# Performance work log

Hardware: AMD Instinct MI355X
Metric: run time of the kernel (lower is better)

Reference implementation:

```python
import jax, jax.numpy as jnp
import numpy as np

# Instant-NGP HashEncoder defaults (torch-ngp) with desired_resolution=2048
L = 16            # num levels
F = 2             # features per level
T = 2 ** 19       # hashmap size per level
BASE = 16         # base resolution
DESIRED = 2048
BOUND = 1.0
PLS = float(np.exp(np.log(DESIRED / BASE) / (L - 1)))
RES = [int(np.ceil(BASE * PLS ** l)) for l in range(L)]  # per-level grid resolution

_OFFS = jnp.array([[i, j, k] for i in range(2) for j in range(2) for k in range(2)], dtype=jnp.uint32)  # [8,3]
_P1 = jnp.uint32(2654435761)
_P2 = jnp.uint32(805459861)


def _level_encode(x01, table, res):
    """x01: [N,3] in [0,1]; table: [T,F]; returns trilinearly-interpolated [N,F]."""
    pos = x01 * res                      # [N,3]
    pf = jnp.floor(pos)
    frac = pos - pf                      # [N,3]
    pi = pf.astype(jnp.uint32)
    corners = pi[:, None, :] + _OFFS[None]  # [N,8,3]
    if (res + 1) ** 3 <= T:
        # dense (collision-free) indexing for coarse levels
        s = jnp.uint32(res + 1)
        idx = corners[..., 0] + s * (corners[..., 1] + s * corners[..., 2])
    else:
        # spatial hash: xor of coordinate * large primes, masked to table size
        idx = (corners[..., 0] ^ (corners[..., 1] * _P1) ^ (corners[..., 2] * _P2)) & jnp.uint32(T - 1)
    # trilinear weights: prod over dims of frac (offset=1) or 1-frac (offset=0)
    w = jnp.prod(jnp.where(_OFFS[None].astype(bool), frac[:, None, :], 1.0 - frac[:, None, :]), axis=-1)  # [N,8]
    return jnp.sum(table[idx] * w[..., None], axis=1)  # [N,F]


def setup_inputs() -> dict:
    key = jax.random.key(0)
    k1, k2, k3, k4 = jax.random.split(key, 4)
    N = 2_097_152
    xyzs = jax.random.uniform(k1, (N, 3), jnp.float32) * 2.0 - 1.0          # in [-bound, bound]
    tables = (jax.random.uniform(k2, (L, T, F), jnp.float32) * 2.0 - 1.0) * 1e-4  # NGP init U(-1e-4,1e-4)
    W1 = jax.random.normal(k3, (L * F, 64), jnp.float32) * (1.0 / np.sqrt(L * F))
    W2 = jax.random.normal(k4, (64, 16), jnp.float32) * (1.0 / np.sqrt(64.0))
    return {"xyzs": xyzs, "tables": tables, "W1": W1, "W2": W2}


def reference(xyzs, tables, W1, W2):
    # normalize to [0,1] using bound (encoder(xyzs, bound))
    x01 = jnp.clip((xyzs + BOUND) / (2.0 * BOUND), 0.0, 1.0)
    enc = jnp.concatenate([_level_encode(x01, tables[l], RES[l]) for l in range(L)], axis=-1)  # [N,32]
    h = jax.nn.relu(enc @ W1)   # [N,64]
    out = h @ W2                # [N,16]
    sigmas = jnp.exp(out[..., 0])   # trunc_exp activation on density channel
    geo_features = out[..., 1:]     # [N,15]
    return sigmas, geo_features
```

## Files before the change

kernel.cpp:

```cpp
#include <hip/hip_runtime.h>
#include <math.h>

#define NLEV 16
#define TSIZE 524288
#define TMASK (TSIZE - 1)
#define P1 2654435761u
#define P2 805459861u

struct ResParams { int res[NLEV]; int dense[NLEV]; };

__device__ __forceinline__ float clamp01f(float v) {
    return fminf(fmaxf(v, 0.0f), 1.0f);
}

__device__ __forceinline__ unsigned f2bf(float f) {
    union { float f; unsigned u; } c; c.f = f;
    return (c.u + 0x7FFFu + ((c.u >> 16) & 1u)) >> 16;
}
__device__ __forceinline__ float bflo(unsigned u) {
    union { unsigned u; float f; } c; c.u = u << 16; return c.f;
}
__device__ __forceinline__ float bfhi(unsigned u) {
    union { unsigned u; float f; } c; c.u = u & 0xFFFF0000u; return c.f;
}

__global__ __launch_bounds__(256) void prep_kernel(
    const float* __restrict__ tables,
    const float* __restrict__ W1,
    const float* __restrict__ W2,
    unsigned* __restrict__ tbl_bf,
    float* __restrict__ W1t,
    float* __restrict__ W2c)
{
    const int t = blockIdx.x * 256 + threadIdx.x;
    const float4 v = *(const float4*)(tables + (size_t)t * 4);
    uint2 o;
    o.x = f2bf(v.x) | (f2bf(v.y) << 16);
    o.y = f2bf(v.z) | (f2bf(v.w) << 16);
    *(uint2*)(tbl_bf + (size_t)t * 2) = o;

    if (blockIdx.x == 0) {
        for (int i = threadIdx.x; i < 2048; i += 256)
            W1t[(i & 63) * 32 + (i >> 6)] = W1[i];
        for (int i = threadIdx.x; i < 1024; i += 256)
            W2c[i] = W2[i];
    }
}

__global__ __launch_bounds__(256) void enc_dense_kernel(
    const float* __restrict__ xyzs,
    const float* __restrict__ tables,
    unsigned* __restrict__ enc_ws,
    ResParams rp, int N)
{
    const int gid = blockIdx.x * 256 + threadIdx.x;
    const float x0 = clamp01f((__builtin_nontemporal_load(xyzs + 3 * gid + 0) + 1.0f) * 0.5f);
    const float y0 = clamp01f((__builtin_nontemporal_load(xyzs + 3 * gid + 1) + 1.0f) * 0.5f);
    const float z0 = clamp01f((__builtin_nontemporal_load(xyzs + 3 * gid + 2) + 1.0f) * 0.5f);
    const float2* tb = (const float2*)tables;

#pragma unroll
    for (int l = 0; l < 5; ++l) {
        const int res = rp.res[l];
        const float rf = (float)res;
        const float px = x0 * rf, py = y0 * rf, pz = z0 * rf;
        const float fx = floorf(px), fy = floorf(py), fz = floorf(pz);
        const float rx = px - fx, ry = py - fy, rz = pz - fz;
        const unsigned ix = (unsigned)fx, iy = (unsigned)fy, iz = (unsigned)fz;

        const unsigned s = (unsigned)(res + 1);
        const unsigned ss = s * s;
        const unsigned base = ix + s * (iy + s * iz);
        unsigned idx[8];
        idx[0] = base;
        idx[1] = base + ss;
        idx[2] = base + s;
        idx[3] = base + s + ss;
        idx[4] = base + 1u;
        idx[5] = base + 1u + ss;
        idx[6] = base + 1u + s;
        idx[7] = base + 1u + s + ss;

        const float2* tl = tb + (size_t)l * TSIZE;
        float2 v[8];
#pragma unroll
        for (int c = 0; c < 8; ++c) v[c] = tl[idx[c]];

        const float wx0 = 1.0f - rx, wy0 = 1.0f - ry, wz0 = 1.0f - rz;
        float e0 = 0.0f, e1 = 0.0f;
#pragma unroll
        for (int c = 0; c < 8; ++c) {
            const float wx = (c & 4) ? rx : wx0;
            const float wy = (c & 2) ? ry : wy0;
            const float wz = (c & 1) ? rz : wz0;
            const float w = (wx * wy) * wz;
            e0 += w * v[c].x;
            e1 += w * v[c].y;
        }
        __builtin_nontemporal_store(f2bf(e0) | (f2bf(e1) << 16),
                                    enc_ws + (size_t)l * N + gid);
    }
}

__global__ __launch_bounds__(256) void enc_hash_kernel(
    const float* __restrict__ xyzs,
    const unsigned* __restrict__ tbl_bf,
    unsigned* __restrict__ enc_ws,
    int level, int res, int N)
{
    const int gid = blockIdx.x * 256 + threadIdx.x;
    const float x0 = clamp01f((__builtin_nontemporal_load(xyzs + 3 * gid + 0) + 1.0f) * 0.5f);
    const float y0 = clamp01f((__builtin_nontemporal_load(xyzs + 3 * gid + 1) + 1.0f) * 0.5f);
    const float z0 = clamp01f((__builtin_nontemporal_load(xyzs + 3 * gid + 2) + 1.0f) * 0.5f);

    const float rf = (float)res;
    const float px = x0 * rf, py = y0 * rf, pz = z0 * rf;
    const float fx = floorf(px), fy = floorf(py), fz = floorf(pz);
    const float rx = px - fx, ry = py - fy, rz = pz - fz;
    const unsigned ix = (unsigned)fx, iy = (unsigned)fy, iz = (unsigned)fz;

    const unsigned ax0 = ix,        ax1 = ix + 1u;
    const unsigned by0 = iy * P1,   by1 = (iy + 1u) * P1;
    const unsigned cz0 = iz * P2,   cz1 = (iz + 1u) * P2;
    unsigned idx[8];
    idx[0] = (ax0 ^ by0 ^ cz0) & TMASK;
    idx[1] = (ax0 ^ by0 ^ cz1) & TMASK;
    idx[2] = (ax0 ^ by1 ^ cz0) & TMASK;
    idx[3] = (ax0 ^ by1 ^ cz1) & TMASK;
    idx[4] = (ax1 ^ by0 ^ cz0) & TMASK;
    idx[5] = (ax1 ^ by0 ^ cz1) & TMASK;
    idx[6] = (ax1 ^ by1 ^ cz0) & TMASK;
    idx[7] = (ax1 ^ by1 ^ cz1) & TMASK;

    const unsigned* tl = tbl_bf + (size_t)level * TSIZE;
    unsigned v[8];
#pragma unroll
    for (int c = 0; c < 8; ++c) v[c] = tl[idx[c]];

    const float wx0 = 1.0f - rx, wy0 = 1.0f - ry, wz0 = 1.0f - rz;
    float e0 = 0.0f, e1 = 0.0f;
#pragma unroll
    for (int c = 0; c < 8; ++c) {
        const float wx = (c & 4) ? rx : wx0;
        const float wy = (c & 2) ? ry : wy0;
        const float wz = (c & 1) ? rz : wz0;
        const float w = (wx * wy) * wz;
        e0 += w * bflo(v[c]);
        e1 += w * bfhi(v[c]);
    }
    __builtin_nontemporal_store(f2bf(e0) | (f2bf(e1) << 16),
                                enc_ws + (size_t)level * N + gid);
}

__global__ __launch_bounds__(256) void mlp_kernel(
    const unsigned* __restrict__ enc_ws,
    const float* __restrict__ W1t,
    const float* __restrict__ W2c,
    float* __restrict__ out_sigma,
    float* __restrict__ out_geo,
    int N)
{
    __shared__ float sGeo[4 * 128 * 15];

    const int tid  = threadIdx.x;
    const int wave = tid >> 6;
    const int lane = tid & 63;
    const int base = blockIdx.x * 512 + wave * 128;
    const int pt0 = base + lane;
    const int pt1 = base + 64 + lane;

    float ea[32], eb[32];
#pragma unroll
    for (int l = 0; l < NLEV; ++l) {
        const unsigned u0 = __builtin_nontemporal_load(enc_ws + (size_t)l * N + pt0);
        const unsigned u1 = __builtin_nontemporal_load(enc_ws + (size_t)l * N + pt1);
        ea[2 * l] = bflo(u0); ea[2 * l + 1] = bfhi(u0);
        eb[2 * l] = bflo(u1); eb[2 * l + 1] = bfhi(u1);
    }

    float oa[16], ob[16];
#pragma unroll
    for (int q = 0; q < 16; ++q) { oa[q] = 0.0f; ob[q] = 0.0f; }

#pragma unroll 4
    for (int j = 0; j < 64; ++j) {
        const float4* wr = (const float4*)(W1t + j * 32);
        float h0 = 0.0f, h1 = 0.0f;
#pragma unroll
        for (int k = 0; k < 8; ++k) {
            const float4 w = wr[k];
            h0 += ea[4 * k + 0] * w.x; h1 += eb[4 * k + 0] * w.x;
            h0 += ea[4 * k + 1] * w.y; h1 += eb[4 * k + 1] * w.y;
            h0 += ea[4 * k + 2] * w.z; h1 += eb[4 * k + 2] * w.z;
            h0 += ea[4 * k + 3] * w.w; h1 += eb[4 * k + 3] * w.w;
        }
        h0 = fmaxf(h0, 0.0f); h1 = fmaxf(h1, 0.0f);
        const float4* w2 = (const float4*)(W2c + j * 16);
#pragma unroll
        for (int q = 0; q < 4; ++q) {
            const float4 w = w2[q];
            oa[4 * q + 0] += h0 * w.x; ob[4 * q + 0] += h1 * w.x;
            oa[4 * q + 1] += h0 * w.y; ob[4 * q + 1] += h1 * w.y;
            oa[4 * q + 2] += h0 * w.z; ob[4 * q + 2] += h1 * w.z;
            oa[4 * q + 3] += h0 * w.w; ob[4 * q + 3] += h1 * w.w;
        }
    }

    out_sigma[pt0] = expf(oa[0]);
    out_sigma[pt1] = expf(ob[0]);

    float* gs = &sGeo[wave * 1920];
#pragma unroll
    for (int q = 1; q < 16; ++q) gs[lane * 15 + (q - 1)] = oa[q];
#pragma unroll
    for (int q = 1; q < 16; ++q) gs[(64 + lane) * 15 + (q - 1)] = ob[q];
    __syncthreads();
    const size_t wbase = (size_t)base * 15;
#pragma unroll
    for (int j = 0; j < 30; ++j)
        out_geo[wbase + (size_t)(j * 64 + lane)] = gs[j * 64 + lane];
}

__global__ __launch_bounds__(256) void hashgrid_fused_kernel(
    const float* __restrict__ xyzs,
    const float* __restrict__ tables,
    const float* __restrict__ W1,
    const float* __restrict__ W2,
    float* __restrict__ out_sigma,
    float* __restrict__ out_geo,
    ResParams rp)
{
    __shared__ float sW1t[64 * 32];
    __shared__ float sW2[64 * 16];
    __shared__ float sGeo[256 * 15];

    const int tid = threadIdx.x;
    for (int i = tid; i < 2048; i += 256) {
        int k = i >> 6, j = i & 63;
        sW1t[j * 32 + k] = W1[i];
    }
    for (int i = tid; i < 1024; i += 256) sW2[i] = W2[i];
    __syncthreads();

    const int gid = blockIdx.x * 256 + tid;
    const float x0 = clamp01f((xyzs[3 * gid + 0] + 1.0f) * 0.5f);
    const float y0 = clamp01f((xyzs[3 * gid + 1] + 1.0f) * 0.5f);
    const float z0 = clamp01f((xyzs[3 * gid + 2] + 1.0f) * 0.5f);

    float enc[32];
    const float2* tb = (const float2*)tables;

#pragma unroll
    for (int l = 0; l < NLEV; ++l) {
        const int res = rp.res[l];
        const float rf = (float)res;
        const float px = x0 * rf, py = y0 * rf, pz = z0 * rf;
        const float fx = floorf(px), fy = floorf(py), fz = floorf(pz);
        const float rx = px - fx, ry = py - fy, rz = pz - fz;
        const unsigned ix = (unsigned)fx, iy = (unsigned)fy, iz = (unsigned)fz;

        unsigned idx[8];
        if (rp.dense[l]) {
            const unsigned s = (unsigned)(res + 1);
            const unsigned ss = s * s;
            const unsigned base = ix + s * (iy + s * iz);
            idx[0] = base;          idx[1] = base + ss;
            idx[2] = base + s;      idx[3] = base + s + ss;
            idx[4] = base + 1u;     idx[5] = base + 1u + ss;
            idx[6] = base + 1u + s; idx[7] = base + 1u + s + ss;
        } else {
            const unsigned ax0 = ix,        ax1 = ix + 1u;
            const unsigned by0 = iy * P1,   by1 = (iy + 1u) * P1;
            const unsigned cz0 = iz * P2,   cz1 = (iz + 1u) * P2;
            idx[0] = (ax0 ^ by0 ^ cz0) & TMASK;
            idx[1] = (ax0 ^ by0 ^ cz1) & TMASK;
            idx[2] = (ax0 ^ by1 ^ cz0) & TMASK;
            idx[3] = (ax0 ^ by1 ^ cz1) & TMASK;
            idx[4] = (ax1 ^ by0 ^ cz0) & TMASK;
            idx[5] = (ax1 ^ by0 ^ cz1) & TMASK;
            idx[6] = (ax1 ^ by1 ^ cz0) & TMASK;
            idx[7] = (ax1 ^ by1 ^ cz1) & TMASK;
        }

        const float2* tl = tb + (size_t)l * TSIZE;
        float2 v[8];
#pragma unroll
        for (int c = 0; c < 8; ++c) v[c] = tl[idx[c]];

        const float wx0 = 1.0f - rx, wy0 = 1.0f - ry, wz0 = 1.0f - rz;
        float e0 = 0.0f, e1 = 0.0f;
#pragma unroll
        for (int c = 0; c < 8; ++c) {
            const float wx = (c & 4) ? rx : wx0;
            const float wy = (c & 2) ? ry : wy0;
            const float wz = (c & 1) ? rz : wz0;
            const float w = (wx * wy) * wz;
            e0 += w * v[c].x;
            e1 += w * v[c].y;
        }
        enc[2 * l]     = e0;
        enc[2 * l + 1] = e1;
    }

    float outv[16];
#pragma unroll
    for (int q = 0; q < 16; ++q) outv[q] = 0.0f;

    for (int j = 0; j < 64; ++j) {
        const float4* wrow = (const float4*)&sW1t[j * 32];
        float hj = 0.0f;
#pragma unroll
        for (int kk = 0; kk < 8; ++kk) {
            const float4 wv = wrow[kk];
            hj += enc[4 * kk + 0] * wv.x;
            hj += enc[4 * kk + 1] * wv.y;
            hj += enc[4 * kk + 2] * wv.z;
            hj += enc[4 * kk + 3] * wv.w;
        }
        hj = fmaxf(hj, 0.0f);
        const float4* w2row = (const float4*)&sW2[j * 16];
#pragma unroll
        for (int qq = 0; qq < 4; ++qq) {
            const float4 w2v = w2row[qq];
            outv[4 * qq + 0] += hj * w2v.x;
            outv[4 * qq + 1] += hj * w2v.y;
            outv[4 * qq + 2] += hj * w2v.z;
            outv[4 * qq + 3] += hj * w2v.w;
        }
    }

    out_sigma[gid] = expf(outv[0]);

    const int wave = tid >> 6;
    const int lane = tid & 63;
    float* gs = &sGeo[wave * 960];
#pragma unroll
    for (int q = 1; q < 16; ++q) gs[lane * 15 + (q - 1)] = outv[q];
    __syncthreads();
    const size_t wbase = (size_t)(blockIdx.x * 256 + wave * 64) * 15;
#pragma unroll
    for (int j = 0; j < 15; ++j)
        out_geo[wbase + (size_t)(j * 64 + lane)] = gs[j * 64 + lane];
}

extern "C" void kernel_launch(void* const* d_in, const int* in_sizes, int n_in,
                              void* d_out, int out_size, void* d_ws, size_t ws_size,
                              hipStream_t stream) {
    const float* xyzs   = (const float*)d_in[0];
    const float* tables = (const float*)d_in[1];
    const float* W1     = (const float*)d_in[2];
    const float* W2     = (const float*)d_in[3];
    float* out = (float*)d_out;

    const int N = in_sizes[0] / 3;

    ResParams rp;
    const double PLS = exp(log(2048.0 / 16.0) / 15.0);
    for (int l = 0; l < NLEV; ++l) {
        const double r = ceil(16.0 * pow(PLS, (double)l));
        rp.res[l] = (int)r;
        const long long s = (long long)r + 1;
        rp.dense[l] = (s * s * s <= (long long)TSIZE) ? 1 : 0;
    }
    bool pattern_ok = true;
    for (int l = 0; l < NLEV; ++l)
        if (rp.dense[l] != (l < 5 ? 1 : 0)) pattern_ok = false;

    float* out_sigma = out;
    float* out_geo   = out + N;

    const size_t encB = (size_t)NLEV * (size_t)N * 4;
    const size_t tblB = (size_t)NLEV * (size_t)TSIZE * 4;
    const size_t w1B  = 2048 * 4, w2B = 1024 * 4;
    const size_t need = encB + tblB + w1B + w2B;

    if (pattern_ok && ws_size >= need) {
        unsigned* enc_ws = (unsigned*)d_ws;
        unsigned* tbl_bf = (unsigned*)((char*)d_ws + encB);
        float*    W1t    = (float*)((char*)d_ws + encB + tblB);
        float*    W2c    = (float*)((char*)d_ws + encB + tblB + w1B);

        prep_kernel<<<dim3((NLEV * TSIZE * 2) / 4 / 256), dim3(256), 0, stream>>>(
            tables, W1, W2, tbl_bf, W1t, W2c);

        const dim3 grid(N / 256), block(256);
        enc_dense_kernel<<<grid, block, 0, stream>>>(xyzs, tables, enc_ws, rp, N);
        for (int l = 5; l < NLEV; ++l)
            enc_hash_kernel<<<grid, block, 0, stream>>>(
                xyzs, tbl_bf, enc_ws, l, rp.res[l], N);

        mlp_kernel<<<dim3(N / 512), block, 0, stream>>>(
            enc_ws, W1t, W2c, out_sigma, out_geo, N);
    } else {
        hashgrid_fused_kernel<<<dim3(N / 256), dim3(256), 0, stream>>>(
            xyzs, tables, W1, W2, out_sigma, out_geo, rp);
    }
}
```

Measured before the change: 1.429 ms.

## Morton-sort points before encoding to improve hash-table gather locality

Adds a counting sort of input points by a 15-bit Morton key (histogram, scan, atomic scatter) so the encoding kernels process spatially coherent points and reuse cached table lines. Dense levels now use a precomputed x-adjacent float4 pair table, halving gather count. Hash kernels process two points per thread. The MLP stages weights in shared memory and scatters outputs through the permutation. This adds sort passes and uncoalesced output writes in exchange for better cache locality on the random gathers.

```diff
diff --git a/kernel.cpp b/kernel.cpp
--- a/kernel.cpp
+++ b/kernel.cpp
@@ -6,13 +6,17 @@
 #define TMASK (TSIZE - 1)
 #define P1 2654435761u
 #define P2 805459861u
-
-struct ResParams { int res[NLEV]; int dense[NLEV]; };
+#define NB 32768
+
+struct Params {
+    int res[NLEV];
+    unsigned ncell[5];
+    unsigned doff[5];
+};
 
 __device__ __forceinline__ float clamp01f(float v) {
     return fminf(fmaxf(v, 0.0f), 1.0f);
 }
-
 __device__ __forceinline__ unsigned f2bf(float f) {
     union { float f; unsigned u; } c; c.f = f;
     return (c.u + 0x7FFFu + ((c.u >> 16) & 1u)) >> 16;
@@ -22,6 +26,16 @@
 }
 __device__ __forceinline__ float bfhi(unsigned u) {
     union { unsigned u; float f; } c; c.u = u & 0xFFFF0000u; return c.f;
+}
+__device__ __forceinline__ unsigned spread5(unsigned v) {
+    return (v & 1u) | ((v & 2u) << 2) | ((v & 4u) << 4) |
+           ((v & 8u) << 6) | ((v & 16u) << 8);
+}
+__device__ __forceinline__ unsigned morton_key(float x0, float y0, float z0) {
+    unsigned kx = min(31u, (unsigned)(x0 * 32.0f));
+    unsigned ky = min(31u, (unsigned)(y0 * 32.0f));
+    unsigned kz = min(31u, (unsigned)(z0 * 32.0f));
+    return spread5(kx) | (spread5(ky) << 1) | (spread5(kz) << 2);
 }
 
 __global__ __launch_bounds__(256) void prep_kernel(
@@ -29,16 +43,21 @@
     const float* __restrict__ W1,
     const float* __restrict__ W2,
     unsigned* __restrict__ tbl_bf,
-    float* __restrict__ W1t,
-    float* __restrict__ W2c)
-{
-    const int t = blockIdx.x * 256 + threadIdx.x;
-    const float4 v = *(const float4*)(tables + (size_t)t * 4);
-    uint2 o;
-    o.x = f2bf(v.x) | (f2bf(v.y) << 16);
-    o.y = f2bf(v.z) | (f2bf(v.w) << 16);
-    *(uint2*)(tbl_bf + (size_t)t * 2) = o;
-
+    float4* __restrict__ dense_pairs,
+    float* __restrict__ W1t, float* __restrict__ W2c,
+    Params rp)
+{
+    const unsigned t = blockIdx.x * 256 + threadIdx.x;
+    const unsigned l = t >> 19, c = t & TMASK;
+    const float2* t2 = (const float2*)tables;
+    if (l >= 5) {
+        const float2 v = t2[(size_t)l * TSIZE + c];
+        tbl_bf[(size_t)(l - 5) * TSIZE + c] = f2bf(v.x) | (f2bf(v.y) << 16);
+    } else if (c < rp.ncell[l]) {
+        const float2 a = t2[(size_t)l * TSIZE + c];
+        const float2 b = t2[(size_t)l * TSIZE + c + 1];
+        dense_pairs[rp.doff[l] + c] = make_float4(a.x, a.y, b.x, b.y);
+    }
     if (blockIdx.x == 0) {
         for (int i = threadIdx.x; i < 2048; i += 256)
             W1t[(i & 63) * 32 + (i >> 6)] = W1[i];
@@ -47,17 +66,62 @@
     }
 }
 
-__global__ __launch_bounds__(256) void enc_dense_kernel(
-    const float* __restrict__ xyzs,
-    const float* __restrict__ tables,
+__global__ __launch_bounds__(256) void zero_kernel(unsigned* __restrict__ hist) {
+    hist[blockIdx.x * 256 + threadIdx.x] = 0u;
+}
+
+__global__ __launch_bounds__(256) void hist_kernel(
+    const float* __restrict__ xyzs, unsigned* __restrict__ hist)
+{
+    const int gid = blockIdx.x * 256 + threadIdx.x;
+    const float x0 = clamp01f((xyzs[3 * gid + 0] + 1.0f) * 0.5f);
+    const float y0 = clamp01f((xyzs[3 * gid + 1] + 1.0f) * 0.5f);
+    const float z0 = clamp01f((xyzs[3 * gid + 2] + 1.0f) * 0.5f);
+    atomicAdd(&hist[morton_key(x0, y0, z0)], 1u);
+}
+
+__global__ __launch_bounds__(1024) void scan_kernel(
+    const unsigned* __restrict__ hist, unsigned* __restrict__ work)
+{
+    __shared__ unsigned part[1024];
+    const int tid = threadIdx.x;
+    unsigned loc[32], s = 0;
+#pragma unroll
+    for (int i = 0; i < 32; ++i) { loc[i] = hist[tid * 32 + i]; s += loc[i]; }
+    part[tid] = s; __syncthreads();
+    for (int st = 1; st < 1024; st <<= 1) {
+        unsigned t = (tid >= st) ? part[tid - st] : 0u;
+        __syncthreads();
+        part[tid] += t;
+        __syncthreads();
+    }
+    unsigned base = (tid == 0) ? 0u : part[tid - 1];
+#pragma unroll
+    for (int i = 0; i < 32; ++i) { work[tid * 32 + i] = base; base += loc[i]; }
+}
+
+__global__ __launch_bounds__(256) void scatter_kernel(
+    const float* __restrict__ xyzs, unsigned* __restrict__ work,
+    float4* __restrict__ sorted, unsigned* __restrict__ perm)
+{
+    const int gid = blockIdx.x * 256 + threadIdx.x;
+    const float x0 = clamp01f((xyzs[3 * gid + 0] + 1.0f) * 0.5f);
+    const float y0 = clamp01f((xyzs[3 * gid + 1] + 1.0f) * 0.5f);
+    const float z0 = clamp01f((xyzs[3 * gid + 2] + 1.0f) * 0.5f);
+    const unsigned pos = atomicAdd(&work[morton_key(x0, y0, z0)], 1u);
+    sorted[pos] = make_float4(x0, y0, z0, 0.0f);
+    perm[pos] = (unsigned)gid;
+}
+
+__global__ __launch_bounds__(256) void enc_dense_sorted(
+    const float4* __restrict__ sorted,
+    const float4* __restrict__ dense_pairs,
     unsigned* __restrict__ enc_ws,
-    ResParams rp, int N)
+    Params rp, int N)
 {
     const int gid = blockIdx.x * 256 + threadIdx.x;
-    const float x0 = clamp01f((__builtin_nontemporal_load(xyzs + 3 * gid + 0) + 1.0f) * 0.5f);
-    const float y0 = clamp01f((__builtin_nontemporal_load(xyzs + 3 * gid + 1) + 1.0f) * 0.5f);
-    const float z0 = clamp01f((__builtin_nontemporal_load(xyzs + 3 * gid + 2) + 1.0f) * 0.5f);
-    const float2* tb = (const float2*)tables;
+    const float4 p = sorted[gid];
+    const float x0 = p.x, y0 = p.y, z0 = p.z;
 
 #pragma unroll
     for (int l = 0; l < 5; ++l) {
@@ -70,104 +134,104 @@
 
         const unsigned s = (unsigned)(res + 1);
         const unsigned ss = s * s;
-        const unsigned base = ix + s * (iy + s * iz);
-        unsigned idx[8];
-        idx[0] = base;
-        idx[1] = base + ss;
-        idx[2] = base + s;
-        idx[3] = base + s + ss;
-        idx[4] = base + 1u;
-        idx[5] = base + 1u + ss;
-        idx[6] = base + 1u + s;
-        idx[7] = base + 1u + s + ss;
-
-        const float2* tl = tb + (size_t)l * TSIZE;
-        float2 v[8];
-#pragma unroll
-        for (int c = 0; c < 8; ++c) v[c] = tl[idx[c]];
+        const unsigned a = ix + s * iy + ss * iz;
+        const float4* dpt = dense_pairs + rp.doff[l];
+        const float4 q00 = dpt[a];
+        const float4 q01 = dpt[a + ss];
+        const float4 q10 = dpt[a + s];
+        const float4 q11 = dpt[a + s + ss];
 
         const float wx0 = 1.0f - rx, wy0 = 1.0f - ry, wz0 = 1.0f - rz;
-        float e0 = 0.0f, e1 = 0.0f;
-#pragma unroll
-        for (int c = 0; c < 8; ++c) {
-            const float wx = (c & 4) ? rx : wx0;
-            const float wy = (c & 2) ? ry : wy0;
-            const float wz = (c & 1) ? rz : wz0;
-            const float w = (wx * wy) * wz;
-            e0 += w * v[c].x;
-            e1 += w * v[c].y;
-        }
+        float e0, e1;
+        e0  = (wx0 * wy0) * wz0 * q00.x;  e1  = (wx0 * wy0) * wz0 * q00.y;
+        e0 += (wx0 * wy0) * rz  * q01.x;  e1 += (wx0 * wy0) * rz  * q01.y;
+        e0 += (wx0 * ry ) * wz0 * q10.x;  e1 += (wx0 * ry ) * wz0 * q10.y;
+        e0 += (wx0 * ry ) * rz  * q11.x;  e1 += (wx0 * ry ) * rz  * q11.y;
+        e0 += (rx  * wy0) * wz0 * q00.z;  e1 += (rx  * wy0) * wz0 * q00.w;
+        e0 += (rx  * wy0) * rz  * q01.z;  e1 += (rx  * wy0) * rz  * q01.w;
+        e0 += (rx  * ry ) * wz0 * q10.z;  e1 += (rx  * ry ) * wz0 * q10.w;
+        e0 += (rx  * ry ) * rz  * q11.z;  e1 += (rx  * ry ) * rz  * q11.w;
+
         __builtin_nontemporal_store(f2bf(e0) | (f2bf(e1) << 16),
                                     enc_ws + (size_t)l * N + gid);
     }
 }
 
-__global__ __launch_bounds__(256) void enc_hash_kernel(
-    const float* __restrict__ xyzs,
+template<int LEVEL>
+__global__ __launch_bounds__(256) void enc_hash_sorted(
+    const float4* __restrict__ sorted,
     const unsigned* __restrict__ tbl_bf,
     unsigned* __restrict__ enc_ws,
-    int level, int res, int N)
-{
-    const int gid = blockIdx.x * 256 + threadIdx.x;
-    const float x0 = clamp01f((__builtin_nontemporal_load(xyzs + 3 * gid + 0) + 1.0f) * 0.5f);
-    const float y0 = clamp01f((__builtin_nontemporal_load(xyzs + 3 * gid + 1) + 1.0f) * 0.5f);
-    const float z0 = clamp01f((__builtin_nontemporal_load(xyzs + 3 * gid + 2) + 1.0f) * 0.5f);
-
+    int res, int N)
+{
+    const int g0 = blockIdx.x * 512 + threadIdx.x;
+    const unsigned* tl = tbl_bf + (size_t)(LEVEL - 5) * TSIZE;
     const float rf = (float)res;
-    const float px = x0 * rf, py = y0 * rf, pz = z0 * rf;
-    const float fx = floorf(px), fy = floorf(py), fz = floorf(pz);
-    const float rx = px - fx, ry = py - fy, rz = pz - fz;
-    const unsigned ix = (unsigned)fx, iy = (unsigned)fy, iz = (unsigned)fz;
-
-    const unsigned ax0 = ix,        ax1 = ix + 1u;
-    const unsigned by0 = iy * P1,   by1 = (iy + 1u) * P1;
-    const unsigned cz0 = iz * P2,   cz1 = (iz + 1u) * P2;
-    unsigned idx[8];
-    idx[0] = (ax0 ^ by0 ^ cz0) & TMASK;
-    idx[1] = (ax0 ^ by0 ^ cz1) & TMASK;
-    idx[2] = (ax0 ^ by1 ^ cz0) & TMASK;
-    idx[3] = (ax0 ^ by1 ^ cz1) & TMASK;
-    idx[4] = (ax1 ^ by0 ^ cz0) & TMASK;
-    idx[5] = (ax1 ^ by0 ^ cz1) & TMASK;
-    idx[6] = (ax1 ^ by1 ^ cz0) & TMASK;
-    idx[7] = (ax1 ^ by1 ^ cz1) & TMASK;
-
-    const unsigned* tl = tbl_bf + (size_t)level * TSIZE;
-    unsigned v[8];
-#pragma unroll
-    for (int c = 0; c < 8; ++c) v[c] = tl[idx[c]];
-
-    const float wx0 = 1.0f - rx, wy0 = 1.0f - ry, wz0 = 1.0f - rz;
-    float e0 = 0.0f, e1 = 0.0f;
-#pragma unroll
-    for (int c = 0; c < 8; ++c) {
-        const float wx = (c & 4) ? rx : wx0;
-        const float wy = (c & 2) ? ry : wy0;
-        const float wz = (c & 1) ? rz : wz0;
-        const float w = (wx * wy) * wz;
-        e0 += w * bflo(v[c]);
-        e1 += w * bfhi(v[c]);
-    }
-    __builtin_nontemporal_store(f2bf(e0) | (f2bf(e1) << 16),
-                                enc_ws + (size_t)level * N + gid);
-}
-
-__global__ __launch_bounds__(256) void mlp_kernel(
+
+    int gid[2] = { g0, g0 + 256 };
+    unsigned v[2][8];
+    float rx[2], ry[2], rz[2];
+
+#pragma unroll
+    for (int p = 0; p < 2; ++p) {
+        const float4 pt = sorted[gid[p]];
+        const float px = pt.x * rf, py = pt.y * rf, pz = pt.z * rf;
+        const float fx = floorf(px), fy = floorf(py), fz = floorf(pz);
+        rx[p] = px - fx; ry[p] = py - fy; rz[p] = pz - fz;
+        const unsigned ix = (unsigned)fx, iy = (unsigned)fy, iz = (unsigned)fz;
+        const unsigned ax0 = ix,        ax1 = ix + 1u;
+        const unsigned by0 = iy * P1,   by1 = (iy + 1u) * P1;
+        const unsigned cz0 = iz * P2,   cz1 = (iz + 1u) * P2;
+        unsigned idx[8];
+        idx[0] = (ax0 ^ by0 ^ cz0) & TMASK;
+        idx[1] = (ax0 ^ by0 ^ cz1) & TMASK;
+        idx[2] = (ax0 ^ by1 ^ cz0) & TMASK;
+        idx[3] = (ax0 ^ by1 ^ cz1) & TMASK;
+        idx[4] = (ax1 ^ by0 ^ cz0) & TMASK;
+        idx[5] = (ax1 ^ by0 ^ cz1) & TMASK;
+        idx[6] = (ax1 ^ by1 ^ cz0) & TMASK;
+        idx[7] = (ax1 ^ by1 ^ cz1) & TMASK;
+#pragma unroll
+        for (int c = 0; c < 8; ++c) v[p][c] = tl[idx[c]];
+    }
+
+#pragma unroll
+    for (int p = 0; p < 2; ++p) {
+        const float wx0 = 1.0f - rx[p], wy0 = 1.0f - ry[p], wz0 = 1.0f - rz[p];
+        float e0 = 0.0f, e1 = 0.0f;
+#pragma unroll
+        for (int c = 0; c < 8; ++c) {
+            const float wx = (c & 4) ? rx[p] : wx0;
+            const float wy = (c & 2) ? ry[p] : wy0;
+            const float wz = (c & 1) ? rz[p] : wz0;
+            const float w = (wx * wy) * wz;
+            e0 += w * bflo(v[p][c]);
+            e1 += w * bfhi(v[p][c]);
+        }
+        __builtin_nontemporal_store(f2bf(e0) | (f2bf(e1) << 16),
+                                    enc_ws + (size_t)LEVEL * N + gid[p]);
+    }
+}
+
+__global__ __launch_bounds__(256) void mlp_scatter_kernel(
     const unsigned* __restrict__ enc_ws,
+    const unsigned* __restrict__ perm,
     const float* __restrict__ W1t,
     const float* __restrict__ W2c,
     float* __restrict__ out_sigma,
     float* __restrict__ out_geo,
     int N)
 {
-    __shared__ float sGeo[4 * 128 * 15];
-
-    const int tid  = threadIdx.x;
-    const int wave = tid >> 6;
-    const int lane = tid & 63;
-    const int base = blockIdx.x * 512 + wave * 128;
-    const int pt0 = base + lane;
-    const int pt1 = base + 64 + lane;
+    __shared__ float sW1t[64 * 32];
+    __shared__ float sW2[64 * 16];
+
+    const int tid = threadIdx.x;
+    for (int i = tid; i < 2048; i += 256) sW1t[i] = W1t[i];
+    for (int i = tid; i < 1024; i += 256) sW2[i] = W2c[i];
+    __syncthreads();
+
+    const int pt0 = blockIdx.x * 512 + tid;
+    const int pt1 = pt0 + 256;
 
     float ea[32], eb[32];
 #pragma unroll
@@ -182,9 +246,8 @@
 #pragma unroll
     for (int q = 0; q < 16; ++q) { oa[q] = 0.0f; ob[q] = 0.0f; }
 
-#pragma unroll 4
     for (int j = 0; j < 64; ++j) {
-        const float4* wr = (const float4*)(W1t + j * 32);
+        const float4* wr = (const float4*)&sW1t[j * 32];
         float h0 = 0.0f, h1 = 0.0f;
 #pragma unroll
         for (int k = 0; k < 8; ++k) {
@@ -195,7 +258,7 @@
             h0 += ea[4 * k + 3] * w.w; h1 += eb[4 * k + 3] * w.w;
         }
         h0 = fmaxf(h0, 0.0f); h1 = fmaxf(h1, 0.0f);
-        const float4* w2 = (const float4*)(W2c + j * 16);
+        const float4* w2 = (const float4*)&sW2[j * 16];
 #pragma unroll
         for (int q = 0; q < 4; ++q) {
             const float4 w = w2[q];
@@ -206,19 +269,16 @@
         }
     }
 
-    out_sigma[pt0] = expf(oa[0]);
-    out_sigma[pt1] = expf(ob[0]);
-
-    float* gs = &sGeo[wave * 1920];
-#pragma unroll
-    for (int q = 1; q < 16; ++q) gs[lane * 15 + (q - 1)] = oa[q];
-#pragma unroll
-    for (int q = 1; q < 16; ++q) gs[(64 + lane) * 15 + (q - 1)] = ob[q];
-    __syncthreads();
-    const size_t wbase = (size_t)base * 15;
-#pragma unroll
-    for (int j = 0; j < 30; ++j)
-        out_geo[wbase + (size_t)(j * 64 + lane)] = gs[j * 64 + lane];
+    const unsigned o0 = perm[pt0];
+    const unsigned o1 = perm[pt1];
+    out_sigma[o0] = expf(oa[0]);
+    out_sigma[o1] = expf(ob[0]);
+#pragma unroll
+    for (int q = 1; q < 16; ++q)
+        out_geo[(size_t)o0 * 15 + (q - 1)] = oa[q];
+#pragma unroll
+    for (int q = 1; q < 16; ++q)
+        out_geo[(size_t)o1 * 15 + (q - 1)] = ob[q];
 }
 
 __global__ __launch_bounds__(256) void hashgrid_fused_kernel(
@@ -228,7 +288,7 @@
     const float* __restrict__ W2,
     float* __restrict__ out_sigma,
     float* __restrict__ out_geo,
-    ResParams rp)
+    Params rp, int ndense)
 {
     __shared__ float sW1t[64 * 32];
     __shared__ float sW2[64 * 16];
@@ -260,7 +320,7 @@
         const unsigned ix = (unsigned)fx, iy = (unsigned)fy, iz = (unsigned)fz;
 
         unsigned idx[8];
-        if (rp.dense[l]) {
+        if (l < ndense) {
             const unsigned s = (unsigned)(res + 1);
             const unsigned ss = s * s;
             const unsigned base = ix + s * (iy + s * iz);
@@ -354,45 +414,80 @@
 
     const int N = in_sizes[0] / 3;
 
-    ResParams rp;
+    Params rp;
+    int ndense = 0;
     const double PLS = exp(log(2048.0 / 16.0) / 15.0);
+    bool pattern_ok = true;
     for (int l = 0; l < NLEV; ++l) {
         const double r = ceil(16.0 * pow(PLS, (double)l));
         rp.res[l] = (int)r;
         const long long s = (long long)r + 1;
-        rp.dense[l] = (s * s * s <= (long long)TSIZE) ? 1 : 0;
-    }
-    bool pattern_ok = true;
-    for (int l = 0; l < NLEV; ++l)
-        if (rp.dense[l] != (l < 5 ? 1 : 0)) pattern_ok = false;
+        const bool dense = (s * s * s <= (long long)TSIZE);
+        if (dense) ndense = l + 1;
+        if (dense != (l < 5)) pattern_ok = false;
+    }
+    unsigned doff = 0;
+    if (pattern_ok) {
+        for (int l = 0; l < 5; ++l) {
+            const unsigned s = (unsigned)rp.res[l] + 1;
+            rp.ncell[l] = s * s * s;
+            rp.doff[l] = doff;
+            doff += rp.ncell[l];
+        }
+    }
 
     float* out_sigma = out;
     float* out_geo   = out + N;
 
-    const size_t encB = (size_t)NLEV * (size_t)N * 4;
-    const size_t tblB = (size_t)NLEV * (size_t)TSIZE * 4;
-    const size_t w1B  = 2048 * 4, w2B = 1024 * 4;
-    const size_t need = encB + tblB + w1B + w2B;
+    const size_t dpB  = (size_t)doff * 16;
+    const size_t srtB = (size_t)N * 16;
+    const size_t encB = (size_t)NLEV * N * 4;
+    const size_t tblB = (size_t)11 * TSIZE * 4;
+    const size_t prmB = (size_t)N * 4;
+    const size_t hstB = (size_t)NB * 4;
+    const size_t need = dpB + srtB + encB + tblB + prmB + 2 * hstB + 3072 * 4;
 
     if (pattern_ok && ws_size >= need) {
-        unsigned* enc_ws = (unsigned*)d_ws;
-        unsigned* tbl_bf = (unsigned*)((char*)d_ws + encB);
-        float*    W1t    = (float*)((char*)d_ws + encB + tblB);
-        float*    W2c    = (float*)((char*)d_ws + encB + tblB + w1B);
-
-        prep_kernel<<<dim3((NLEV * TSIZE * 2) / 4 / 256), dim3(256), 0, stream>>>(
-            tables, W1, W2, tbl_bf, W1t, W2c);
-
-        const dim3 grid(N / 256), block(256);
-        enc_dense_kernel<<<grid, block, 0, stream>>>(xyzs, tables, enc_ws, rp, N);
-        for (int l = 5; l < NLEV; ++l)
-            enc_hash_kernel<<<grid, block, 0, stream>>>(
-                xyzs, tbl_bf, enc_ws, l, rp.res[l], N);
-
-        mlp_kernel<<<dim3(N / 512), block, 0, stream>>>(
-            enc_ws, W1t, W2c, out_sigma, out_geo, N);
+        char* w = (char*)d_ws;
+        float4*   dense_pairs = (float4*)w;              w += dpB;
+        float4*   sorted      = (float4*)w;              w += srtB;
+        unsigned* enc_ws      = (unsigned*)w;            w += encB;
+        unsigned* tbl_bf      = (unsigned*)w;            w += tblB;
+        unsigned* perm        = (unsigned*)w;            w += prmB;
+        unsigned* hist        = (unsigned*)w;            w += hstB;
+        unsigned* work        = (unsigned*)w;            w += hstB;
+        float*    W1t         = (float*)w;               w += 2048 * 4;
+        float*    W2c         = (float*)w;
+
+        prep_kernel<<<dim3(NLEV * TSIZE / 256), dim3(256), 0, stream>>>(
+            tables, W1, W2, tbl_bf, dense_pairs, W1t, W2c, rp);
+
+        zero_kernel<<<dim3(NB / 256), dim3(256), 0, stream>>>(hist);
+        hist_kernel<<<dim3(N / 256), dim3(256), 0, stream>>>(xyzs, hist);
+        scan_kernel<<<dim3(1), dim3(1024), 0, stream>>>(hist, work);
+        scatter_kernel<<<dim3(N / 256), dim3(256), 0, stream>>>(
+            xyzs, work, sorted, perm);
+
+        enc_dense_sorted<<<dim3(N / 256), dim3(256), 0, stream>>>(
+            sorted, dense_pairs, enc_ws, rp, N);
+
+        const dim3 g2(N / 512), blk(256);
+        enc_hash_sorted< 5><<<g2, blk, 0, stream>>>(sorted, tbl_bf, enc_ws, rp.res[ 5], N);
+        enc_hash_sorted< 6><<<g2, blk, 0, stream>>>(sorted, tbl_bf, enc_ws, rp.res[ 6], N);
+        enc_hash_sorted< 7><<<g2, blk, 0, stream>>>(sorted, tbl_bf, enc_ws, rp.res[ 7], N);
+        enc_hash_sorted< 8><<<g2, blk, 0, stream>>>(sorted, tbl_bf, enc_ws, rp.res[ 8], N);
+        enc_hash_sorted< 9><<<g2, blk, 0, stream>>>(sorted, tbl_bf, enc_ws, rp.res[ 9], N);
+        enc_hash_sorted<10><<<g2, blk, 0, stream>>>(sorted, tbl_bf, enc_ws, rp.res[10], N);
+        enc_hash_sorted<11><<<g2, blk, 0, stream>>>(sorted, tbl_bf, enc_ws, rp.res[11], N);
+        enc_hash_sorted<12><<<g2, blk, 0, stream>>>(sorted, tbl_bf, enc_ws, rp.res[12], N);
+        enc_hash_sorted<13><<<g2, blk, 0, stream>>>(sorted, tbl_bf, enc_ws, rp.res[13], N);
+        enc_hash_sorted<14><<<g2, blk, 0, stream>>>(sorted, tbl_bf, enc_ws, rp.res[14], N);
+        enc_hash_sorted<15><<<g2, blk, 0, stream>>>(sorted, tbl_bf, enc_ws, rp.res[15], N);
+
+        mlp_scatter_kernel<<<dim3(N / 512), blk, 0, stream>>>(
+            enc_ws, perm, W1t, W2c, out_sigma, out_geo, N);
     } else {
         hashgrid_fused_kernel<<<dim3(N / 256), dim3(256), 0, stream>>>(
-            xyzs, tables, W1, W2, out_sigma, out_geo, rp);
-    }
-}
+            xyzs, tables, W1, W2, out_sigma, out_geo, rp, ndense);
+    }
+}
```

Result: faster. 1.233 ms (-13.7%).
